# Kernel optimization log

Measured on AMD Instinct MI355X. Metric: run time of the kernel, lower is better.

The kernel has to match this reference:

```python
import jax, jax.numpy as jnp
import numpy as np

DIM = 1024
HEADS = 16
DIM_HEAD = 64


def setup_inputs() -> dict:
    key = jax.random.key(0)
    k1, k2 = jax.random.split(key)
    x = jax.random.normal(k1, (2, 2048, DIM), dtype=jnp.float32)
    # to_qkv: Linear(dim, 3*heads*dim_head, bias=False); torch weight is [out,in],
    # we store the transposed [in,out] form for x @ W.
    W_qkv = jax.random.normal(k2, (DIM, 3 * HEADS * DIM_HEAD), dtype=jnp.float32) * (DIM ** -0.5)
    return {"x": x, "W_qkv": W_qkv}


def reference(x, W_qkv):
    b, n, _ = x.shape
    h, d = HEADS, DIM_HEAD
    scale = d ** -0.5
    qkv = x @ W_qkv                              # [b, n, 3*h*d]
    q, k, v = jnp.split(qkv, 3, axis=-1)
    # 'b n (h d) -> b h n d'
    q = q.reshape(b, n, h, d).transpose(0, 2, 1, 3)
    k = k.reshape(b, n, h, d).transpose(0, 2, 1, 3)
    v = v.reshape(b, n, h, d).transpose(0, 2, 1, 3)
    dots = jnp.einsum('bhnd,bhmd->bhnm', q, k) * scale
    attn = jax.nn.softmax(dots, axis=-1)
    out = jnp.einsum('bhnm,bhmd->bhnd', attn, v)
    out = out.transpose(0, 2, 1, 3).reshape(b, n, h * d)  # 'b h n d -> b n (h d)'
    return out + x  # residual (to_out is never applied in the source forward)
```

## Files before the change

kernel.cpp:

```cpp
#include <hip/hip_runtime.h>

#define DIM   1024
#define NQKV  3072
#define SEQ   2048
#define HEADS 16
#define DHEAD 64
#define M_TOT 4096

typedef __bf16 bf16;
typedef __bf16 bf16x8 __attribute__((ext_vector_type(8)));
typedef float  f32x4  __attribute__((ext_vector_type(4)));

typedef const __attribute__((address_space(1))) unsigned int gu32;
typedef __attribute__((address_space(3))) unsigned int su32;

static __device__ __forceinline__ unsigned short f2b(float f) {
    bf16 h = (bf16)f;
    return __builtin_bit_cast(unsigned short, h);
}

#define CAST_BLOCKS (M_TOT * DIM / (256 * 4))
#define TR_NB (NQKV / 64)
__global__ void prep_kernel(const float* __restrict__ x,
                            unsigned short* __restrict__ xb,
                            const float* __restrict__ W,
                            unsigned short* __restrict__ Wt) {
    __shared__ float tile[64][65];
    const int id  = blockIdx.x;
    const int tid = threadIdx.x;
    if (id < CAST_BLOCKS) {
        int i = (id * 256 + tid) * 4;
        float4 v = *(const float4*)(x + i);
        ushort4 o;
        o.x = f2b(v.x); o.y = f2b(v.y); o.z = f2b(v.z); o.w = f2b(v.w);
        *(ushort4*)(xb + i) = o;
    } else {
        int t  = id - CAST_BLOCKS;
        int nb = t % TR_NB;
        int kb = t / TR_NB;
        #pragma unroll
        for (int p = 0; p < 4; p++) {
            int kl = p * 16 + (tid >> 4);
            int nl = (tid & 15) * 4;
            float4 v = *(const float4*)&W[(size_t)(kb * 64 + kl) * NQKV + nb * 64 + nl];
            tile[nl + 0][kl] = v.x;
            tile[nl + 1][kl] = v.y;
            tile[nl + 2][kl] = v.z;
            tile[nl + 3][kl] = v.w;
        }
        __syncthreads();
        #pragma unroll
        for (int p = 0; p < 2; p++) {
            int nl = p * 32 + (tid >> 3);
            int k8 = (tid & 7) * 8;
            int n  = nb * 64 + nl;
            float s = (n < 1024) ? 0.18033688f : 1.0f;
            float4 a = *(const float4*)&tile[nl][k8];
            float4 b = *(const float4*)&tile[nl][k8 + 4];
            ushort4 o0, o1;
            o0.x = f2b(a.x * s); o0.y = f2b(a.y * s); o0.z = f2b(a.z * s); o0.w = f2b(a.w * s);
            o1.x = f2b(b.x * s); o1.y = f2b(b.y * s); o1.z = f2b(b.z * s); o1.w = f2b(b.w * s);
            uint4 pk;
            pk.x = ((unsigned)o0.y << 16) | o0.x;
            pk.y = ((unsigned)o0.w << 16) | o0.z;
            pk.z = ((unsigned)o1.y << 16) | o1.x;
            pk.w = ((unsigned)o1.w << 16) | o1.z;
            *(uint4*)&Wt[(size_t)n * DIM + kb * 64 + k8] = pk;
        }
    }
}

#define LDC 136
__global__ __launch_bounds__(256) void qkv_gemm_kernel(
    const unsigned short* __restrict__ A,
    const unsigned short* __restrict__ Bt,
    unsigned short* __restrict__ Qw,
    unsigned short* __restrict__ Kw,
    unsigned short* __restrict__ Vtw)
{
    __shared__ __align__(16) unsigned char smem[128 * LDC * 2];
    unsigned short* As = (unsigned short*)smem;
    unsigned short* Bs = (unsigned short*)(smem + 16384);
    unsigned short* Cs = (unsigned short*)smem;

    const int tid  = threadIdx.x;
    const int m0   = blockIdx.y * 128;
    const int n0   = blockIdx.x * 128;
    const int w    = tid >> 6;
    const int lane = tid & 63;
    const int l16  = lane & 15;
    const int quad = lane >> 4;
    const int wm   = (w >> 1) * 64;
    const int wn   = (w & 1) * 64;
    const int srow = lane >> 3;
    const int scol = (lane & 7) * 8;

    f32x4 acc[4][4];
    const f32x4 fzero = {0.f, 0.f, 0.f, 0.f};
    for (int i = 0; i < 4; i++)
        for (int j = 0; j < 4; j++) acc[i][j] = fzero;

    const unsigned short* Ag = A  + (size_t)(m0 + w * 32 + srow) * DIM + scol;
    const unsigned short* Bg = Bt + (size_t)(n0 + w * 32 + srow) * DIM + scol;

    for (int kt = 0; kt < DIM; kt += 64) {
        #pragma unroll
        for (int j = 0; j < 4; j++) {
            __builtin_amdgcn_global_load_lds((gu32*)(Ag + kt + (size_t)j * 8 * DIM),
                                             (su32*)&As[(w * 32 + j * 8) * 64], 16, 0, 0);
            __builtin_amdgcn_global_load_lds((gu32*)(Bg + kt + (size_t)j * 8 * DIM),
                                             (su32*)&Bs[(w * 32 + j * 8) * 64], 16, 0, 0);
        }
        __syncthreads();
        #pragma unroll
        for (int s = 0; s < 2; s++) {
            bf16x8 af[4], bfr[4];
            #pragma unroll
            for (int i = 0; i < 4; i++) {
                af[i]  = *(const bf16x8*)(&As[(wm + i * 16 + l16) * 64 + s * 32 + quad * 8]);
                bfr[i] = *(const bf16x8*)(&Bs[(wn + i * 16 + l16) * 64 + s * 32 + quad * 8]);
            }
            #pragma unroll
            for (int i = 0; i < 4; i++)
                #pragma unroll
                for (int j = 0; j < 4; j++)
                    acc[i][j] = __builtin_amdgcn_mfma_f32_16x16x32_bf16(af[i], bfr[j], acc[i][j], 0, 0, 0);
        }
        __syncthreads();
    }

    const int part = n0 >> 10;
    const int h0   = (n0 & 1023) >> 6;
    const int b    = m0 >> 11;
    const int np0  = m0 & 2047;

    if (part < 2) {
        #pragma unroll
        for (int i = 0; i < 4; i++)
            #pragma unroll
            for (int j = 0; j < 4; j++)
                #pragma unroll
                for (int r = 0; r < 4; r++)
                    Cs[(wm + i * 16 + quad * 4 + r) * LDC + wn + j * 16 + l16] = f2b(acc[i][j][r]);
        __syncthreads();
        unsigned short* dst = (part == 0) ? Qw : Kw;
        #pragma unroll
        for (int pass = 0; pass < 8; pass++) {
            int mi = pass * 16 + (tid >> 4);
            int ci = (tid & 15) * 8;
            uint4 v = *(const uint4*)&Cs[mi * LDC + ci];
            int bh = b * HEADS + h0 + (ci >> 6);
            *(uint4*)&dst[((size_t)bh * SEQ + np0 + mi) * DHEAD + (ci & 63)] = v;
        }
    } else {
        #pragma unroll
        for (int i = 0; i < 4; i++)
            #pragma unroll
            for (int j = 0; j < 4; j++) {
                ushort4 pk;
                pk.x = f2b(acc[i][j][0]); pk.y = f2b(acc[i][j][1]);
                pk.z = f2b(acc[i][j][2]); pk.w = f2b(acc[i][j][3]);
                *(ushort4*)&Cs[(wn + j * 16 + l16) * LDC + wm + i * 16 + quad * 4] = pk;
            }
        __syncthreads();
        #pragma unroll
        for (int pass = 0; pass < 8; pass++) {
            int ci = pass * 16 + (tid >> 4);
            int mi = (tid & 15) * 8;
            uint4 v = *(const uint4*)&Cs[ci * LDC + mi];
            int bh = b * HEADS + h0 + (ci >> 6);
            *(uint4*)&Vtw[((size_t)bh * DHEAD + (ci & 63)) * SEQ + np0 + mi] = v;
        }
    }
}

#define LDK 72
__global__ __launch_bounds__(256) void attn_kernel(
    const unsigned short* __restrict__ Qw,
    const unsigned short* __restrict__ Kw,
    const unsigned short* __restrict__ Vtw,
    const float* __restrict__ x,
    float* __restrict__ out)
{
    __shared__ __align__(16) unsigned short Ks[2][64 * LDK];
    __shared__ __align__(16) unsigned short Vs[2][64 * LDK];
    const int id  = blockIdx.x;
    const int qt  = id >> 5;
    const int bh  = ((id & 7) << 2) | ((id >> 3) & 3);
    const int tid = threadIdx.x;
    const int w   = tid >> 6, lane = tid & 63;
    const int l16 = lane & 15, quad = lane >> 4;

    const unsigned short* Qb = Qw + ((size_t)bh * SEQ + qt * 128 + w * 32 + l16) * DHEAD;
    bf16x8 qf[2][2];
    #pragma unroll
    for (int qh = 0; qh < 2; qh++) {
        qf[qh][0] = *(const bf16x8*)(Qb + qh * 16 * DHEAD + quad * 8);
        qf[qh][1] = *(const bf16x8*)(Qb + qh * 16 * DHEAD + 32 + quad * 8);
    }

    bf16x8 ones;
    #pragma unroll
    for (int j = 0; j < 8; j++) ones[j] = (bf16)1.0f;

    f32x4 o[2][4], dsum[2];
    const f32x4 fzero = {0.f, 0.f, 0.f, 0.f};
    #pragma unroll
    for (int qh = 0; qh < 2; qh++) {
        #pragma unroll
        for (int d = 0; d < 4; d++) o[qh][d] = fzero;
        dsum[qh] = fzero;
    }

    const unsigned short* Kg = Kw  + (size_t)bh * SEQ * DHEAD;
    const unsigned short* Vg = Vtw + (size_t)bh * DHEAD * SEQ;

    const int r0 = tid >> 3, c0 = (tid & 7) * 8;
    const int pr0 = ((r0 >> 2) & 1) * 16 + ((r0 >> 3) & 3) * 4 + (r0 & 3);

    uint4 kreg0 = *(const uint4*)(Kg + (size_t)r0 * DHEAD + c0);
    uint4 kreg1 = *(const uint4*)(Kg + (size_t)(r0 + 32) * DHEAD + c0);
    uint4 vreg0 = *(const uint4*)(Vg + (size_t)r0 * SEQ + c0);
    uint4 vreg1 = *(const uint4*)(Vg + (size_t)(r0 + 32) * SEQ + c0);
    *(uint4*)&Ks[0][pr0 * LDK + c0]        = kreg0;
    *(uint4*)&Ks[0][(pr0 + 32) * LDK + c0] = kreg1;
    *(uint4*)&Vs[0][r0 * LDK + c0]         = vreg0;
    *(uint4*)&Vs[0][(r0 + 32) * LDK + c0]  = vreg1;
    kreg0 = *(const uint4*)(Kg + (size_t)(64 + r0) * DHEAD + c0);
    kreg1 = *(const uint4*)(Kg + (size_t)(64 + r0 + 32) * DHEAD + c0);
    vreg0 = *(const uint4*)(Vg + (size_t)r0 * SEQ + 64 + c0);
    vreg1 = *(const uint4*)(Vg + (size_t)(r0 + 32) * SEQ + 64 + c0);

    for (int t = 0; t < SEQ / 64; t++) {
        const int cur = t & 1, nxt = cur ^ 1;
        __syncthreads();
        *(uint4*)&Ks[nxt][pr0 * LDK + c0]        = kreg0;
        *(uint4*)&Ks[nxt][(pr0 + 32) * LDK + c0] = kreg1;
        *(uint4*)&Vs[nxt][r0 * LDK + c0]         = vreg0;
        *(uint4*)&Vs[nxt][(r0 + 32) * LDK + c0]  = vreg1;
        int kvn = ((t + 2) & (SEQ / 64 - 1)) * 64;
        kreg0 = *(const uint4*)(Kg + (size_t)(kvn + r0) * DHEAD + c0);
        kreg1 = *(const uint4*)(Kg + (size_t)(kvn + r0 + 32) * DHEAD + c0);
        vreg0 = *(const uint4*)(Vg + (size_t)r0 * SEQ + kvn + c0);
        vreg1 = *(const uint4*)(Vg + (size_t)(r0 + 32) * SEQ + kvn + c0);

        f32x4 sacc[2][4];
        #pragma unroll
        for (int qh = 0; qh < 2; qh++)
            #pragma unroll
            for (int ki = 0; ki < 4; ki++) sacc[qh][ki] = fzero;
        #pragma unroll
        for (int s = 0; s < 2; s++)
            #pragma unroll
            for (int ki = 0; ki < 4; ki++) {
                bf16x8 kf = *(const bf16x8*)(
                    &Ks[cur][(ki * 16 + l16) * LDK + s * 32 + quad * 8]);
                sacc[0][ki] = __builtin_amdgcn_mfma_f32_16x16x32_bf16(kf, qf[0][s], sacc[0][ki], 0, 0, 0);
                sacc[1][ki] = __builtin_amdgcn_mfma_f32_16x16x32_bf16(kf, qf[1][s], sacc[1][ki], 0, 0, 0);
            }

        bf16x8 pf[2][2];
        #pragma unroll
        for (int qh = 0; qh < 2; qh++)
            #pragma unroll
            for (int s = 0; s < 2; s++)
                #pragma unroll
                for (int half = 0; half < 2; half++) {
                    int ki = 2 * s + half;
                    #pragma unroll
                    for (int r = 0; r < 4; r++)
                        pf[qh][s][half * 4 + r] = (bf16)__builtin_amdgcn_exp2f(sacc[qh][ki][r]);
                }

        #pragma unroll
        for (int s = 0; s < 2; s++) {
            dsum[0] = __builtin_amdgcn_mfma_f32_16x16x32_bf16(pf[0][s], ones, dsum[0], 0, 0, 0);
            dsum[1] = __builtin_amdgcn_mfma_f32_16x16x32_bf16(pf[1][s], ones, dsum[1], 0, 0, 0);
            #pragma unroll
            for (int d = 0; d < 4; d++) {
                bf16x8 vf = *(const bf16x8*)(&Vs[cur][(d * 16 + l16) * LDK + s * 32 + quad * 8]);
                o[0][d] = __builtin_amdgcn_mfma_f32_16x16x32_bf16(pf[0][s], vf, o[0][d], 0, 0, 0);
                o[1][d] = __builtin_amdgcn_mfma_f32_16x16x32_bf16(pf[1][s], vf, o[1][d], 0, 0, 0);
            }
        }
    }

    const int b = bh >> 4, h = bh & 15;
    #pragma unroll
    for (int qh = 0; qh < 2; qh++) {
        float lr[4];
        #pragma unroll
        for (int r = 0; r < 4; r++) lr[r] = __builtin_amdgcn_rcpf(dsum[qh][r]);
        #pragma unroll
        for (int di = 0; di < 4; di++)
            #pragma unroll
            for (int r = 0; r < 4; r++) {
                int np  = qt * 128 + w * 32 + qh * 16 + quad * 4 + r;
                int col = h * 64 + di * 16 + l16;
                size_t g = ((size_t)(b * SEQ + np)) * DIM + col;
                out[g] = o[qh][di][r] * lr[r] + x[g];
            }
    }
}

extern "C" void kernel_launch(void* const* d_in, const int* in_sizes, int n_in,
                              void* d_out, int out_size, void* d_ws, size_t ws_size,
                              hipStream_t stream) {
    const float* x  = (const float*)d_in[0];
    const float* Wq = (const float*)d_in[1];
    float* out = (float*)d_out;

    unsigned short* xb = (unsigned short*)d_ws;
    unsigned short* Wt = xb + (size_t)M_TOT * DIM;
    unsigned short* Qw = Wt + (size_t)NQKV * DIM;
    unsigned short* Kw = Qw + (size_t)32 * SEQ * DHEAD;
    unsigned short* Vt = Kw + (size_t)32 * SEQ * DHEAD;

    prep_kernel<<<CAST_BLOCKS + TR_NB * (DIM / 64), 256, 0, stream>>>(x, xb, Wq, Wt);
    qkv_gemm_kernel<<<dim3(NQKV / 128, M_TOT / 128), 256, 0, stream>>>(xb, Wt, Qw, Kw, Vt);
    attn_kernel<<<(SEQ / 128) * 32, 256, 0, stream>>>(Qw, Kw, Vt, x, out);
}
```

Baseline: 172.9 us.

## Split attention KV sequence across wave pairs with 64-row query tiles per wave

Each wave now handles 64 query rows instead of 32, and the four waves form two pairs that each process half of the key/value sequence, loading two KV tiles per stage. At the end the partial outputs and row sums from the second pair are combined through shared memory before normalisation and the residual add. The aim is to reuse each K and V fragment read from shared memory across more MFMAs. The cost is higher register pressure from doubled accumulators, larger shared memory use, and an extra reduction step.

```diff
diff --git a/kernel.cpp b/kernel.cpp
--- a/kernel.cpp
+++ b/kernel.cpp
@@ -175,6 +175,8 @@
 }
 
 #define LDK 72
+#define TILE_E (64 * LDK)
+#define KT 16
 __global__ __launch_bounds__(256) void attn_kernel(
     const unsigned short* __restrict__ Qw,
     const unsigned short* __restrict__ Kw,
@@ -182,19 +184,24 @@
     const float* __restrict__ x,
     float* __restrict__ out)
 {
-    __shared__ __align__(16) unsigned short Ks[2][64 * LDK];
-    __shared__ __align__(16) unsigned short Vs[2][64 * LDK];
+    __shared__ __align__(16) unsigned char smem[TILE_E * 8 * 2];
+    unsigned short* Ks = (unsigned short*)smem;
+    unsigned short* Vs = (unsigned short*)(smem + TILE_E * 4 * 2);
+    float* scratch = (float*)smem;
+
     const int id  = blockIdx.x;
     const int qt  = id >> 5;
     const int bh  = ((id & 7) << 2) | ((id >> 3) & 3);
     const int tid = threadIdx.x;
     const int w   = tid >> 6, lane = tid & 63;
     const int l16 = lane & 15, quad = lane >> 4;
-
-    const unsigned short* Qb = Qw + ((size_t)bh * SEQ + qt * 128 + w * 32 + l16) * DHEAD;
-    bf16x8 qf[2][2];
+    const int g   = w & 1;
+    const int p   = w >> 1;
+
+    const unsigned short* Qb = Qw + ((size_t)bh * SEQ + qt * 128 + g * 64 + l16) * DHEAD;
+    bf16x8 qf[4][2];
     #pragma unroll
-    for (int qh = 0; qh < 2; qh++) {
+    for (int qh = 0; qh < 4; qh++) {
         qf[qh][0] = *(const bf16x8*)(Qb + qh * 16 * DHEAD + quad * 8);
         qf[qh][1] = *(const bf16x8*)(Qb + qh * 16 * DHEAD + 32 + quad * 8);
     }
@@ -203,10 +210,10 @@
     #pragma unroll
     for (int j = 0; j < 8; j++) ones[j] = (bf16)1.0f;
 
-    f32x4 o[2][4], dsum[2];
+    f32x4 o[4][4], dsum[4];
     const f32x4 fzero = {0.f, 0.f, 0.f, 0.f};
     #pragma unroll
-    for (int qh = 0; qh < 2; qh++) {
+    for (int qh = 0; qh < 4; qh++) {
         #pragma unroll
         for (int d = 0; d < 4; d++) o[qh][d] = fzero;
         dsum[qh] = fzero;
@@ -218,50 +225,71 @@
     const int r0 = tid >> 3, c0 = (tid & 7) * 8;
     const int pr0 = ((r0 >> 2) & 1) * 16 + ((r0 >> 3) & 3) * 4 + (r0 & 3);
 
-    uint4 kreg0 = *(const uint4*)(Kg + (size_t)r0 * DHEAD + c0);
-    uint4 kreg1 = *(const uint4*)(Kg + (size_t)(r0 + 32) * DHEAD + c0);
-    uint4 vreg0 = *(const uint4*)(Vg + (size_t)r0 * SEQ + c0);
-    uint4 vreg1 = *(const uint4*)(Vg + (size_t)(r0 + 32) * SEQ + c0);
-    *(uint4*)&Ks[0][pr0 * LDK + c0]        = kreg0;
-    *(uint4*)&Ks[0][(pr0 + 32) * LDK + c0] = kreg1;
-    *(uint4*)&Vs[0][r0 * LDK + c0]         = vreg0;
-    *(uint4*)&Vs[0][(r0 + 32) * LDK + c0]  = vreg1;
-    kreg0 = *(const uint4*)(Kg + (size_t)(64 + r0) * DHEAD + c0);
-    kreg1 = *(const uint4*)(Kg + (size_t)(64 + r0 + 32) * DHEAD + c0);
-    vreg0 = *(const uint4*)(Vg + (size_t)r0 * SEQ + 64 + c0);
-    vreg1 = *(const uint4*)(Vg + (size_t)(r0 + 32) * SEQ + 64 + c0);
-
-    for (int t = 0; t < SEQ / 64; t++) {
+    uint4 k00 = *(const uint4*)(Kg + (size_t)r0 * DHEAD + c0);
+    uint4 k01 = *(const uint4*)(Kg + (size_t)(r0 + 32) * DHEAD + c0);
+    uint4 k10 = *(const uint4*)(Kg + (size_t)(1024 + r0) * DHEAD + c0);
+    uint4 k11 = *(const uint4*)(Kg + (size_t)(1024 + r0 + 32) * DHEAD + c0);
+    uint4 v00 = *(const uint4*)(Vg + (size_t)r0 * SEQ + c0);
+    uint4 v01 = *(const uint4*)(Vg + (size_t)(r0 + 32) * SEQ + c0);
+    uint4 v10 = *(const uint4*)(Vg + (size_t)r0 * SEQ + 1024 + c0);
+    uint4 v11 = *(const uint4*)(Vg + (size_t)(r0 + 32) * SEQ + 1024 + c0);
+    *(uint4*)&Ks[0 * TILE_E + pr0 * LDK + c0]        = k00;
+    *(uint4*)&Ks[0 * TILE_E + (pr0 + 32) * LDK + c0] = k01;
+    *(uint4*)&Ks[1 * TILE_E + pr0 * LDK + c0]        = k10;
+    *(uint4*)&Ks[1 * TILE_E + (pr0 + 32) * LDK + c0] = k11;
+    *(uint4*)&Vs[0 * TILE_E + r0 * LDK + c0]         = v00;
+    *(uint4*)&Vs[0 * TILE_E + (r0 + 32) * LDK + c0]  = v01;
+    *(uint4*)&Vs[1 * TILE_E + r0 * LDK + c0]         = v10;
+    *(uint4*)&Vs[1 * TILE_E + (r0 + 32) * LDK + c0]  = v11;
+    k00 = *(const uint4*)(Kg + (size_t)(64 + r0) * DHEAD + c0);
+    k01 = *(const uint4*)(Kg + (size_t)(64 + r0 + 32) * DHEAD + c0);
+    k10 = *(const uint4*)(Kg + (size_t)(1024 + 64 + r0) * DHEAD + c0);
+    k11 = *(const uint4*)(Kg + (size_t)(1024 + 64 + r0 + 32) * DHEAD + c0);
+    v00 = *(const uint4*)(Vg + (size_t)r0 * SEQ + 64 + c0);
+    v01 = *(const uint4*)(Vg + (size_t)(r0 + 32) * SEQ + 64 + c0);
+    v10 = *(const uint4*)(Vg + (size_t)r0 * SEQ + 1024 + 64 + c0);
+    v11 = *(const uint4*)(Vg + (size_t)(r0 + 32) * SEQ + 1024 + 64 + c0);
+
+    for (int t = 0; t < KT; t++) {
         const int cur = t & 1, nxt = cur ^ 1;
         __syncthreads();
-        *(uint4*)&Ks[nxt][pr0 * LDK + c0]        = kreg0;
-        *(uint4*)&Ks[nxt][(pr0 + 32) * LDK + c0] = kreg1;
-        *(uint4*)&Vs[nxt][r0 * LDK + c0]         = vreg0;
-        *(uint4*)&Vs[nxt][(r0 + 32) * LDK + c0]  = vreg1;
-        int kvn = ((t + 2) & (SEQ / 64 - 1)) * 64;
-        kreg0 = *(const uint4*)(Kg + (size_t)(kvn + r0) * DHEAD + c0);
-        kreg1 = *(const uint4*)(Kg + (size_t)(kvn + r0 + 32) * DHEAD + c0);
-        vreg0 = *(const uint4*)(Vg + (size_t)r0 * SEQ + kvn + c0);
-        vreg1 = *(const uint4*)(Vg + (size_t)(r0 + 32) * SEQ + kvn + c0);
-
-        f32x4 sacc[2][4];
-        #pragma unroll
-        for (int qh = 0; qh < 2; qh++)
+        *(uint4*)&Ks[(nxt * 2 + 0) * TILE_E + pr0 * LDK + c0]        = k00;
+        *(uint4*)&Ks[(nxt * 2 + 0) * TILE_E + (pr0 + 32) * LDK + c0] = k01;
+        *(uint4*)&Ks[(nxt * 2 + 1) * TILE_E + pr0 * LDK + c0]        = k10;
+        *(uint4*)&Ks[(nxt * 2 + 1) * TILE_E + (pr0 + 32) * LDK + c0] = k11;
+        *(uint4*)&Vs[(nxt * 2 + 0) * TILE_E + r0 * LDK + c0]         = v00;
+        *(uint4*)&Vs[(nxt * 2 + 0) * TILE_E + (r0 + 32) * LDK + c0]  = v01;
+        *(uint4*)&Vs[(nxt * 2 + 1) * TILE_E + r0 * LDK + c0]         = v10;
+        *(uint4*)&Vs[(nxt * 2 + 1) * TILE_E + (r0 + 32) * LDK + c0]  = v11;
+        int kvn = ((t + 2) & (KT - 1)) * 64;
+        k00 = *(const uint4*)(Kg + (size_t)(kvn + r0) * DHEAD + c0);
+        k01 = *(const uint4*)(Kg + (size_t)(kvn + r0 + 32) * DHEAD + c0);
+        k10 = *(const uint4*)(Kg + (size_t)(1024 + kvn + r0) * DHEAD + c0);
+        k11 = *(const uint4*)(Kg + (size_t)(1024 + kvn + r0 + 32) * DHEAD + c0);
+        v00 = *(const uint4*)(Vg + (size_t)r0 * SEQ + kvn + c0);
+        v01 = *(const uint4*)(Vg + (size_t)(r0 + 32) * SEQ + kvn + c0);
+        v10 = *(const uint4*)(Vg + (size_t)r0 * SEQ + 1024 + kvn + c0);
+        v11 = *(const uint4*)(Vg + (size_t)(r0 + 32) * SEQ + 1024 + kvn + c0);
+
+        const unsigned short* Kb = Ks + (size_t)(cur * 2 + p) * TILE_E;
+        f32x4 sacc[4][4];
+        #pragma unroll
+        for (int qh = 0; qh < 4; qh++)
             #pragma unroll
             for (int ki = 0; ki < 4; ki++) sacc[qh][ki] = fzero;
         #pragma unroll
         for (int s = 0; s < 2; s++)
             #pragma unroll
             for (int ki = 0; ki < 4; ki++) {
-                bf16x8 kf = *(const bf16x8*)(
-                    &Ks[cur][(ki * 16 + l16) * LDK + s * 32 + quad * 8]);
-                sacc[0][ki] = __builtin_amdgcn_mfma_f32_16x16x32_bf16(kf, qf[0][s], sacc[0][ki], 0, 0, 0);
-                sacc[1][ki] = __builtin_amdgcn_mfma_f32_16x16x32_bf16(kf, qf[1][s], sacc[1][ki], 0, 0, 0);
+                bf16x8 kf = *(const bf16x8*)(&Kb[(ki * 16 + l16) * LDK + s * 32 + quad * 8]);
+                #pragma unroll
+                for (int qh = 0; qh < 4; qh++)
+                    sacc[qh][ki] = __builtin_amdgcn_mfma_f32_16x16x32_bf16(kf, qf[qh][s], sacc[qh][ki], 0, 0, 0);
             }
 
-        bf16x8 pf[2][2];
-        #pragma unroll
-        for (int qh = 0; qh < 2; qh++)
+        bf16x8 pf[4][2];
+        #pragma unroll
+        for (int qh = 0; qh < 4; qh++)
             #pragma unroll
             for (int s = 0; s < 2; s++)
                 #pragma unroll
@@ -272,34 +300,59 @@
                         pf[qh][s][half * 4 + r] = (bf16)__builtin_amdgcn_exp2f(sacc[qh][ki][r]);
                 }
 
+        const unsigned short* Vb = Vs + (size_t)(cur * 2 + p) * TILE_E;
         #pragma unroll
         for (int s = 0; s < 2; s++) {
-            dsum[0] = __builtin_amdgcn_mfma_f32_16x16x32_bf16(pf[0][s], ones, dsum[0], 0, 0, 0);
-            dsum[1] = __builtin_amdgcn_mfma_f32_16x16x32_bf16(pf[1][s], ones, dsum[1], 0, 0, 0);
+            #pragma unroll
+            for (int qh = 0; qh < 4; qh++)
+                dsum[qh] = __builtin_amdgcn_mfma_f32_16x16x32_bf16(pf[qh][s], ones, dsum[qh], 0, 0, 0);
             #pragma unroll
             for (int d = 0; d < 4; d++) {
-                bf16x8 vf = *(const bf16x8*)(&Vs[cur][(d * 16 + l16) * LDK + s * 32 + quad * 8]);
-                o[0][d] = __builtin_amdgcn_mfma_f32_16x16x32_bf16(pf[0][s], vf, o[0][d], 0, 0, 0);
-                o[1][d] = __builtin_amdgcn_mfma_f32_16x16x32_bf16(pf[1][s], vf, o[1][d], 0, 0, 0);
+                bf16x8 vf = *(const bf16x8*)(&Vb[(d * 16 + l16) * LDK + s * 32 + quad * 8]);
+                #pragma unroll
+                for (int qh = 0; qh < 4; qh++)
+                    o[qh][d] = __builtin_amdgcn_mfma_f32_16x16x32_bf16(pf[qh][s], vf, o[qh][d], 0, 0, 0);
             }
         }
     }
 
-    const int b = bh >> 4, h = bh & 15;
-    #pragma unroll
-    for (int qh = 0; qh < 2; qh++) {
-        float lr[4];
-        #pragma unroll
-        for (int r = 0; r < 4; r++) lr[r] = __builtin_amdgcn_rcpf(dsum[qh][r]);
-        #pragma unroll
-        for (int di = 0; di < 4; di++)
-            #pragma unroll
-            for (int r = 0; r < 4; r++) {
-                int np  = qt * 128 + w * 32 + qh * 16 + quad * 4 + r;
-                int col = h * 64 + di * 16 + l16;
-                size_t g = ((size_t)(b * SEQ + np)) * DIM + col;
-                out[g] = o[qh][di][r] * lr[r] + x[g];
-            }
+    __syncthreads();
+    if (w >= 2) {
+        float* sc = scratch + ((size_t)((w - 2) * 64 + lane)) * 84;
+        #pragma unroll
+        for (int qh = 0; qh < 4; qh++) {
+            #pragma unroll
+            for (int di = 0; di < 4; di++)
+                *(f32x4*)(sc + (qh * 4 + di) * 4) = o[qh][di];
+            *(f32x4*)(sc + 64 + qh * 4) = dsum[qh];
+        }
+    }
+    __syncthreads();
+    if (w < 2) {
+        float* sc = scratch + ((size_t)(w * 64 + lane)) * 84;
+        #pragma unroll
+        for (int qh = 0; qh < 4; qh++) {
+            #pragma unroll
+            for (int di = 0; di < 4; di++)
+                o[qh][di] += *(const f32x4*)(sc + (qh * 4 + di) * 4);
+            dsum[qh] += *(const f32x4*)(sc + 64 + qh * 4);
+        }
+        const int b = bh >> 4, h = bh & 15;
+        #pragma unroll
+        for (int qh = 0; qh < 4; qh++) {
+            float lr[4];
+            #pragma unroll
+            for (int r = 0; r < 4; r++) lr[r] = __builtin_amdgcn_rcpf(dsum[qh][r]);
+            #pragma unroll
+            for (int di = 0; di < 4; di++)
+                #pragma unroll
+                for (int r = 0; r < 4; r++) {
+                    int np  = qt * 128 + g * 64 + qh * 16 + quad * 4 + r;
+                    int col = h * 64 + di * 16 + l16;
+                    size_t gidx = ((size_t)(b * SEQ + np)) * DIM + col;
+                    out[gidx] = o[qh][di][r] * lr[r] + x[gidx];
+                }
+        }
     }
 }
 
```

Result: slower. 181.1 us (+4.8%).

## Split attention KV range across two wave groups with direct global-to-LDS loads

Applied to the files above, without the earlier changes.

Attention blocks now use 512 threads: two groups of four waves each process half of the key sequence (split-K) for the same 128 queries, and their partial outputs and row sums are combined through LDS at the end. K/V tiles are loaded straight into LDS with global_load_lds using an XOR-swizzled layout in place of padded rows and register staging, and the loop drops double buffering, using two barriers per iteration. The aim is more waves per block to hide latency and to cut register and LDS staging cost. In exchange there is an extra reduction step, more barriers, and no overlap between loads and compute inside a block.

```diff
diff --git a/kernel.cpp b/kernel.cpp
--- a/kernel.cpp
+++ b/kernel.cpp
@@ -174,24 +174,30 @@
     }
 }
 
-#define LDK 72
-__global__ __launch_bounds__(256) void attn_kernel(
+#define KT 16
+__global__ __launch_bounds__(512, 4) void attn_kernel(
     const unsigned short* __restrict__ Qw,
     const unsigned short* __restrict__ Kw,
     const unsigned short* __restrict__ Vtw,
     const float* __restrict__ x,
     float* __restrict__ out)
 {
-    __shared__ __align__(16) unsigned short Ks[2][64 * LDK];
-    __shared__ __align__(16) unsigned short Vs[2][64 * LDK];
+    __shared__ __align__(16) unsigned char smem[32768];
+    unsigned short* KsU = (unsigned short*)smem;
+    unsigned short* VsU = KsU + 8192;
+    float* scratch = (float*)smem;
+
     const int id  = blockIdx.x;
     const int qt  = id >> 5;
     const int bh  = ((id & 7) << 2) | ((id >> 3) & 3);
     const int tid = threadIdx.x;
     const int w   = tid >> 6, lane = tid & 63;
     const int l16 = lane & 15, quad = lane >> 4;
-
-    const unsigned short* Qb = Qw + ((size_t)bh * SEQ + qt * 128 + w * 32 + l16) * DHEAD;
+    const int g   = w & 3;
+    const int p   = w >> 2;
+    const int xq  = l16 & 7;
+
+    const unsigned short* Qb = Qw + ((size_t)bh * SEQ + qt * 128 + g * 32 + l16) * DHEAD;
     bf16x8 qf[2][2];
     #pragma unroll
     for (int qh = 0; qh < 2; qh++) {
@@ -215,34 +221,28 @@
     const unsigned short* Kg = Kw  + (size_t)bh * SEQ * DHEAD;
     const unsigned short* Vg = Vtw + (size_t)bh * DHEAD * SEQ;
 
-    const int r0 = tid >> 3, c0 = (tid & 7) * 8;
-    const int pr0 = ((r0 >> 2) & 1) * 16 + ((r0 >> 3) & 3) * 4 + (r0 & 3);
-
-    uint4 kreg0 = *(const uint4*)(Kg + (size_t)r0 * DHEAD + c0);
-    uint4 kreg1 = *(const uint4*)(Kg + (size_t)(r0 + 32) * DHEAD + c0);
-    uint4 vreg0 = *(const uint4*)(Vg + (size_t)r0 * SEQ + c0);
-    uint4 vreg1 = *(const uint4*)(Vg + (size_t)(r0 + 32) * SEQ + c0);
-    *(uint4*)&Ks[0][pr0 * LDK + c0]        = kreg0;
-    *(uint4*)&Ks[0][(pr0 + 32) * LDK + c0] = kreg1;
-    *(uint4*)&Vs[0][r0 * LDK + c0]         = vreg0;
-    *(uint4*)&Vs[0][(r0 + 32) * LDK + c0]  = vreg1;
-    kreg0 = *(const uint4*)(Kg + (size_t)(64 + r0) * DHEAD + c0);
-    kreg1 = *(const uint4*)(Kg + (size_t)(64 + r0 + 32) * DHEAD + c0);
-    vreg0 = *(const uint4*)(Vg + (size_t)r0 * SEQ + 64 + c0);
-    vreg1 = *(const uint4*)(Vg + (size_t)(r0 + 32) * SEQ + 64 + c0);
-
-    for (int t = 0; t < SEQ / 64; t++) {
-        const int cur = t & 1, nxt = cur ^ 1;
-        __syncthreads();
-        *(uint4*)&Ks[nxt][pr0 * LDK + c0]        = kreg0;
-        *(uint4*)&Ks[nxt][(pr0 + 32) * LDK + c0] = kreg1;
-        *(uint4*)&Vs[nxt][r0 * LDK + c0]         = vreg0;
-        *(uint4*)&Vs[nxt][(r0 + 32) * LDK + c0]  = vreg1;
-        int kvn = ((t + 2) & (SEQ / 64 - 1)) * 64;
-        kreg0 = *(const uint4*)(Kg + (size_t)(kvn + r0) * DHEAD + c0);
-        kreg1 = *(const uint4*)(Kg + (size_t)(kvn + r0 + 32) * DHEAD + c0);
-        vreg0 = *(const uint4*)(Vg + (size_t)r0 * SEQ + kvn + c0);
-        vreg1 = *(const uint4*)(Vg + (size_t)(r0 + 32) * SEQ + kvn + c0);
+    const int sl   = lane >> 3;
+    const int c16s = (lane & 7) ^ sl;
+    const int pr   = 8 * w + sl;
+    const int rlog = ((pr >> 2) & 3) * 8 + ((pr >> 4) & 1) * 4 + (pr & 3) + (pr & 32);
+    const size_t koff = (size_t)rlog * DHEAD + c16s * 8;
+    const size_t voff = (size_t)pr * SEQ + c16s * 8;
+
+    for (int t = 0; t < KT; t++) {
+        __syncthreads();
+        const size_t kb = (size_t)(t * 64) * DHEAD;
+        __builtin_amdgcn_global_load_lds((gu32*)(Kg + kb + koff),
+                                         (su32*)&KsU[w * 512], 16, 0, 0);
+        __builtin_amdgcn_global_load_lds((gu32*)(Kg + kb + (size_t)1024 * DHEAD + koff),
+                                         (su32*)&KsU[4096 + w * 512], 16, 0, 0);
+        __builtin_amdgcn_global_load_lds((gu32*)(Vg + voff + t * 64),
+                                         (su32*)&VsU[w * 512], 16, 0, 0);
+        __builtin_amdgcn_global_load_lds((gu32*)(Vg + voff + 1024 + t * 64),
+                                         (su32*)&VsU[4096 + w * 512], 16, 0, 0);
+        __syncthreads();
+
+        const unsigned short* Kb = KsU + p * 4096;
+        const unsigned short* Vb = VsU + p * 4096;
 
         f32x4 sacc[2][4];
         #pragma unroll
@@ -250,14 +250,15 @@
             #pragma unroll
             for (int ki = 0; ki < 4; ki++) sacc[qh][ki] = fzero;
         #pragma unroll
-        for (int s = 0; s < 2; s++)
+        for (int s = 0; s < 2; s++) {
+            const int col = ((s * 4 + quad) ^ xq) * 8;
             #pragma unroll
             for (int ki = 0; ki < 4; ki++) {
-                bf16x8 kf = *(const bf16x8*)(
-                    &Ks[cur][(ki * 16 + l16) * LDK + s * 32 + quad * 8]);
+                bf16x8 kf = *(const bf16x8*)(&Kb[(ki * 16 + l16) * 64 + col]);
                 sacc[0][ki] = __builtin_amdgcn_mfma_f32_16x16x32_bf16(kf, qf[0][s], sacc[0][ki], 0, 0, 0);
                 sacc[1][ki] = __builtin_amdgcn_mfma_f32_16x16x32_bf16(kf, qf[1][s], sacc[1][ki], 0, 0, 0);
             }
+        }
 
         bf16x8 pf[2][2];
         #pragma unroll
@@ -274,32 +275,56 @@
 
         #pragma unroll
         for (int s = 0; s < 2; s++) {
+            const int col = ((s * 4 + quad) ^ xq) * 8;
             dsum[0] = __builtin_amdgcn_mfma_f32_16x16x32_bf16(pf[0][s], ones, dsum[0], 0, 0, 0);
             dsum[1] = __builtin_amdgcn_mfma_f32_16x16x32_bf16(pf[1][s], ones, dsum[1], 0, 0, 0);
             #pragma unroll
             for (int d = 0; d < 4; d++) {
-                bf16x8 vf = *(const bf16x8*)(&Vs[cur][(d * 16 + l16) * LDK + s * 32 + quad * 8]);
+                bf16x8 vf = *(const bf16x8*)(&Vb[(d * 16 + l16) * 64 + col]);
                 o[0][d] = __builtin_amdgcn_mfma_f32_16x16x32_bf16(pf[0][s], vf, o[0][d], 0, 0, 0);
                 o[1][d] = __builtin_amdgcn_mfma_f32_16x16x32_bf16(pf[1][s], vf, o[1][d], 0, 0, 0);
             }
         }
     }
 
-    const int b = bh >> 4, h = bh & 15;
+    __syncthreads();
     #pragma unroll
-    for (int qh = 0; qh < 2; qh++) {
-        float lr[4];
-        #pragma unroll
-        for (int r = 0; r < 4; r++) lr[r] = __builtin_amdgcn_rcpf(dsum[qh][r]);
-        #pragma unroll
-        for (int di = 0; di < 4; di++)
-            #pragma unroll
-            for (int r = 0; r < 4; r++) {
-                int np  = qt * 128 + w * 32 + qh * 16 + quad * 4 + r;
-                int col = h * 64 + di * 16 + l16;
-                size_t g = ((size_t)(b * SEQ + np)) * DIM + col;
-                out[g] = o[qh][di][r] * lr[r] + x[g];
-            }
+    for (int ch = 0; ch < 2; ch++) {
+        if (ch) __syncthreads();
+        if (p == 1) {
+            float* sc = scratch + ((size_t)(g * 64 + lane)) * 20;
+            #pragma unroll
+            for (int di = 0; di < 4; di++)
+                *(f32x4*)(sc + di * 4) = o[ch][di];
+            *(f32x4*)(sc + 16) = dsum[ch];
+        }
+        __syncthreads();
+        if (p == 0) {
+            float* sc = scratch + ((size_t)(g * 64 + lane)) * 20;
+            #pragma unroll
+            for (int di = 0; di < 4; di++)
+                o[ch][di] += *(const f32x4*)(sc + di * 4);
+            dsum[ch] += *(const f32x4*)(sc + 16);
+        }
+    }
+
+    if (p == 0) {
+        const int b = bh >> 4, h = bh & 15;
+        #pragma unroll
+        for (int ch = 0; ch < 2; ch++) {
+            float lr[4];
+            #pragma unroll
+            for (int r = 0; r < 4; r++) lr[r] = __builtin_amdgcn_rcpf(dsum[ch][r]);
+            #pragma unroll
+            for (int di = 0; di < 4; di++)
+                #pragma unroll
+                for (int r = 0; r < 4; r++) {
+                    int np  = qt * 128 + g * 32 + ch * 16 + quad * 4 + r;
+                    int col = h * 64 + di * 16 + l16;
+                    size_t gidx = ((size_t)(b * SEQ + np)) * DIM + col;
+                    out[gidx] = o[ch][di][r] * lr[r] + x[gidx];
+                }
+        }
     }
 }
 
@@ -318,5 +343,5 @@
 
     prep_kernel<<<CAST_BLOCKS + TR_NB * (DIM / 64), 256, 0, stream>>>(x, xb, Wq, Wt);
     qkv_gemm_kernel<<<dim3(NQKV / 128, M_TOT / 128), 256, 0, stream>>>(xb, Wt, Qw, Kw, Vt);
-    attn_kernel<<<(SEQ / 128) * 32, 256, 0, stream>>>(Qw, Kw, Vt, x, out);
-}
+    attn_kernel<<<(SEQ / 128) * 32, 512, 0, stream>>>(Qw, Kw, Vt, x, out);
+}
```

New measurement: 160.0 us. 7.4% less time.
